# Kernel optimization log

Measured on AMD Instinct MI355X. Metric: run time of the kernel, lower is better.

The kernel has to match this reference:

```python
import jax, jax.numpy as jnp
import numpy as np

H_IN = 7
W_IN = 7
SIZE_CHANNEL = 524288


def setup_inputs() -> dict:
    key = jax.random.key(0)
    k1, k2, k3 = jax.random.split(key, 3)
    x = jax.random.normal(k1, (1, SIZE_CHANNEL, H_IN, W_IN), dtype=jnp.float32)
    weight = jax.random.normal(k2, (H_IN * W_IN, SIZE_CHANNEL), dtype=jnp.float32)
    bias = jax.random.normal(k3, (H_IN * W_IN, SIZE_CHANNEL), dtype=jnp.float32)
    return {"x": x, "weight": weight, "bias": bias}


def reference(x, weight, bias):
    # x: (1, C, 7, 7). Replicate swapaxes(1,3) + flatten(end_dim=2) -> (49, C)
    B, C, H, W = x.shape
    xf = jnp.transpose(x, (0, 3, 2, 1)).reshape(B * W * H, C)  # (49, C)
    # Per-channel 7x7 matmul, fully batched over channels:
    Xc = xf.T.reshape(C, H_IN, W_IN)           # (C, 7, 7)
    Wc = weight.T.reshape(C, H_IN, W_IN)       # (C, 7, 7)
    prod = jnp.einsum('cij,cjk->cik', Xc, Wc)  # (C, 7, 7)
    out = prod.reshape(C, H_IN * W_IN).T + bias  # (49, C)
    return out
```

## Files before the change

### kernel.cpp

```cpp
#include <hip/hip_runtime.h>


typedef float f4 __attribute__((ext_vector_type(4)));

constexpr int C    = 524288;
constexpr int HW   = 49;
constexpr int CHB  = 256;
constexpr int NTHR = 64 * 7;
constexpr int RS   = CHB;
constexpr int NF4  = CHB * HW / 4;

__global__ __launch_bounds__(NTHR)
void mylinear_kernel(const float* __restrict__ x,
                     const float* __restrict__ w,
                     const float* __restrict__ b,
                     float* __restrict__ out) {
    __shared__ float xs[HW * CHB];

    const int tid   = threadIdx.y * 64 + threadIdx.x;
    const int cbase = blockIdx.x * CHB;

    const f4* __restrict__ xsrc = reinterpret_cast<const f4*>(x + (size_t)cbase * HW);
#pragma unroll
    for (int it = 0; it < NF4 / NTHR; ++it) {
        const int idx = it * NTHR + tid;
        const f4 v = xsrc[idx];
#pragma unroll
        for (int t = 0; t < 4; ++t) {
            const int e   = idx * 4 + t;
            const int cl  = e / HW;
            const int pos = e % HW;
            const int g   = (pos >> 2) & 7;
            const int sl  = (cl >> 2) ^ g;
            xs[pos * RS + (sl << 2 | (cl & 3))] = v[t];
        }
    }
    __syncthreads();

    const int q  = threadIdx.x;
    const int kk = threadIdx.y;
    const int c  = cbase + (q << 2);

    f4 wq[7];
#pragma unroll
    for (int j = 0; j < 7; ++j)
        wq[j] = *reinterpret_cast<const f4*>(w + (size_t)(j * 7 + kk) * C + c);

    f4 bcur = *reinterpret_cast<const f4*>(b + (size_t)(0 * 7 + kk) * C + c);

#pragma unroll
    for (int i = 0; i < 7; ++i) {
        f4 bnext;
        if (i < 6)
            bnext = *reinterpret_cast<const f4*>(b + (size_t)((i + 1) * 7 + kk) * C + c);

        f4 xv[7];
#pragma unroll
        for (int j = 0; j < 7; ++j) {
            const int pos = j * 7 + i;
            const int g   = (pos >> 2) & 7;
            xv[j] = *reinterpret_cast<const f4*>(xs + pos * RS + ((q ^ g) << 2));
        }
        f4 acc = bcur;
#pragma unroll
        for (int j = 0; j < 7; ++j) {
            acc.x = fmaf(xv[j].x, wq[j].x, acc.x);
            acc.y = fmaf(xv[j].y, wq[j].y, acc.y);
            acc.z = fmaf(xv[j].z, wq[j].z, acc.z);
            acc.w = fmaf(xv[j].w, wq[j].w, acc.w);
        }
        __builtin_nontemporal_store(acc,
            reinterpret_cast<f4*>(out + (size_t)(i * 7 + kk) * C + c));
        bcur = bnext;
    }
}

extern "C" void kernel_launch(void* const* d_in, const int* in_sizes, int n_in,
                              void* d_out, int out_size, void* d_ws, size_t ws_size,
                              hipStream_t stream) {
    const float* x = (const float*)d_in[0];
    const float* w = (const float*)d_in[1];
    const float* b = (const float*)d_in[2];
    float* out     = (float*)d_out;

    dim3 grid(C / CHB), block(64, 7);
    mylinear_kernel<<<grid, block, 0, stream>>>(x, w, b, out);
}
```

Measured before the change: 72.18 us.

## Halve channels per block and switch to float2 vectors for occupancy

Reduces the channel tile per block from 256 to 128 and has each thread handle two channels with float2 loads and stores instead of four with float4. This halves shared memory per block and doubles the grid, and adds a min-blocks launch bound so more blocks can be resident to hide memory latency. The LDS swizzle is reworked for 2-wide slots. The cost is narrower global transactions (8-byte instead of 16-byte per thread) and more blocks, each repeating the staging overhead.

```diff
diff --git a/kernel.cpp b/kernel.cpp
--- a/kernel.cpp
+++ b/kernel.cpp
@@ -2,15 +2,16 @@
 
 
 typedef float f4 __attribute__((ext_vector_type(4)));
+typedef float f2 __attribute__((ext_vector_type(2)));
 
 constexpr int C    = 524288;
 constexpr int HW   = 49;
-constexpr int CHB  = 256;
+constexpr int CHB  = 128;
 constexpr int NTHR = 64 * 7;
 constexpr int RS   = CHB;
-constexpr int NF4  = CHB * HW / 4;
+constexpr int NF2  = CHB * HW / 2;
 
-__global__ __launch_bounds__(NTHR)
+__global__ __launch_bounds__(NTHR, 7)
 void mylinear_kernel(const float* __restrict__ x,
                      const float* __restrict__ w,
                      const float* __restrict__ b,
@@ -20,57 +21,54 @@
     const int tid   = threadIdx.y * 64 + threadIdx.x;
     const int cbase = blockIdx.x * CHB;
 
-    const f4* __restrict__ xsrc = reinterpret_cast<const f4*>(x + (size_t)cbase * HW);
+    const f2* __restrict__ xsrc = reinterpret_cast<const f2*>(x + (size_t)cbase * HW);
 #pragma unroll
-    for (int it = 0; it < NF4 / NTHR; ++it) {
+    for (int it = 0; it < NF2 / NTHR; ++it) {
         const int idx = it * NTHR + tid;
-        const f4 v = xsrc[idx];
+        const f2 v = xsrc[idx];
 #pragma unroll
-        for (int t = 0; t < 4; ++t) {
-            const int e   = idx * 4 + t;
+        for (int t = 0; t < 2; ++t) {
+            const int e   = idx * 2 + t;
             const int cl  = e / HW;
             const int pos = e % HW;
-            const int g   = (pos >> 2) & 7;
-            const int sl  = (cl >> 2) ^ g;
-            xs[pos * RS + (sl << 2 | (cl & 3))] = v[t];
+            const int sl  = (cl >> 1) ^ (pos & 31);
+            xs[pos * RS + (sl << 1 | (cl & 1))] = v[t];
         }
     }
     __syncthreads();
 
     const int q  = threadIdx.x;
     const int kk = threadIdx.y;
-    const int c  = cbase + (q << 2);
+    const int c  = cbase + (q << 1);
 
-    f4 wq[7];
+    f2 wq[7];
 #pragma unroll
     for (int j = 0; j < 7; ++j)
-        wq[j] = *reinterpret_cast<const f4*>(w + (size_t)(j * 7 + kk) * C + c);
+        wq[j] = *reinterpret_cast<const f2*>(w + (size_t)(j * 7 + kk) * C + c);
 
-    f4 bcur = *reinterpret_cast<const f4*>(b + (size_t)(0 * 7 + kk) * C + c);
+    f2 bcur = *reinterpret_cast<const f2*>(b + (size_t)kk * C + c);
 
 #pragma unroll
     for (int i = 0; i < 7; ++i) {
-        f4 bnext;
+        f2 bnext;
         if (i < 6)
-            bnext = *reinterpret_cast<const f4*>(b + (size_t)((i + 1) * 7 + kk) * C + c);
+            bnext = *reinterpret_cast<const f2*>(b + (size_t)((i + 1) * 7 + kk) * C + c);
 
-        f4 xv[7];
+        f2 xv[7];
 #pragma unroll
         for (int j = 0; j < 7; ++j) {
             const int pos = j * 7 + i;
-            const int g   = (pos >> 2) & 7;
-            xv[j] = *reinterpret_cast<const f4*>(xs + pos * RS + ((q ^ g) << 2));
+            const int sl  = q ^ (pos & 31);
+            xv[j] = *reinterpret_cast<const f2*>(xs + pos * RS + (sl << 1));
         }
-        f4 acc = bcur;
+        f2 acc = bcur;
 #pragma unroll
         for (int j = 0; j < 7; ++j) {
             acc.x = fmaf(xv[j].x, wq[j].x, acc.x);
             acc.y = fmaf(xv[j].y, wq[j].y, acc.y);
-            acc.z = fmaf(xv[j].z, wq[j].z, acc.z);
-            acc.w = fmaf(xv[j].w, wq[j].w, acc.w);
         }
         __builtin_nontemporal_store(acc,
-            reinterpret_cast<f4*>(out + (size_t)(i * 7 + kk) * C + c));
+            reinterpret_cast<f2*>(out + (size_t)(i * 7 + kk) * C + c));
         bcur = bnext;
     }
 }
```

Result: slower. 80.82 us (+12.0%).
